# Kernel optimization log

Hardware: AMD Instinct MI355X
Metric: run time of the kernel (lower is better)

The kernel has to match this reference:

```python
import jax, jax.numpy as jnp
import numpy as np

N_CLASSES = 256
GT_CLASSES = 21
DIM = 384
EPS = 1e-12  # matches torch F.normalize default eps


def setup_inputs() -> dict:
    key = jax.random.key(0)
    k1, k2, k3 = jax.random.split(key, 3)
    features = jax.random.normal(k1, (4, 256, 256, DIM), dtype=jnp.float32)
    weight = jax.random.uniform(k2, (4, 256, 256), dtype=jnp.float32)
    cluster_centers = jax.random.normal(k3, (N_CLASSES, DIM), dtype=jnp.float32)
    pseudo_assignment = (jnp.arange(N_CLASSES) % GT_CLASSES).astype(jnp.int32)
    return {
        "features": features,
        "weight": weight,
        "cluster_centers": cluster_centers,
        "pseudo_assignment": pseudo_assignment,
    }


def _l2norm(x, axis):
    # torch F.normalize: x / max(||x||, eps)
    n = jnp.sqrt(jnp.sum(x * x, axis=axis, keepdims=True))
    return x / jnp.maximum(n, EPS)


def reference(features, weight, cluster_centers, pseudo_assignment):
    lead_shape = features.shape[:-1]
    feats = features.reshape(-1, features.shape[-1])        # [N, D]
    w = weight.reshape(-1)                                   # [N]

    normed_clusters = _l2norm(cluster_centers, axis=1)       # [K, D]
    normed_features = _l2norm(feats, axis=1)                 # [N, D]

    inner_products = normed_features @ normed_clusters.T     # [N, K]
    class_labels = jnp.argmax(inner_products, axis=1)        # [N]

    # -(one_hot(labels) * inner_products).sum(1) == -inner_products[n, labels[n]]
    cluster_loss = -jnp.take_along_axis(
        inner_products, class_labels[:, None], axis=1
    )[:, 0]                                                  # [N]

    loss = jnp.mean(cluster_loss * w)

    pseudo_segs_pred = class_labels.reshape(lead_shape)
    segs_pred = pseudo_assignment[pseudo_segs_pred].astype(jnp.int64)
    return pseudo_segs_pred, segs_pred, loss
```

## Files before the change

### kernel.cpp

```cpp
#include <hip/hip_runtime.h>
#include <hip/hip_bf16.h>

#define NTOT (4*256*256)
#define DIM 384
#define KCL 256
#define BM 64
#define TBS 256
#define GRID_MAIN (NTOT/BM)
#define NT 12
#define EPS 1e-12f

#define AB(p) ((p) * 8192)
#define SMEM_BYTES 16384

typedef __attribute__((ext_vector_type(8))) _Float16 f16x8;
typedef __attribute__((ext_vector_type(4))) float f32x4;

__global__ void prep_clusters(const float* __restrict__ cc,
                              _Float16* __restrict__ bh,
                              _Float16* __restrict__ bl) {
    int j = blockIdx.x, l = threadIdx.x;
    float v[6]; float ssq = 0.f;
#pragma unroll
    for (int i = 0; i < 6; ++i) { v[i] = cc[j*DIM + l + 64*i]; ssq = fmaf(v[i], v[i], ssq); }
#pragma unroll
    for (int off = 32; off >= 1; off >>= 1) ssq += __shfl_xor(ssq, off);
    float inv = 1.f / fmaxf(sqrtf(ssq), EPS);
    const int w = j >> 6, n = (j >> 4) & 3, nl = j & 15;
#pragma unroll
    for (int i = 0; i < 6; ++i) {
        int d = l + 64 * i;
        float x = v[i] * inv;
        _Float16 h  = (_Float16)x;
        _Float16 lo = (_Float16)(x - (float)h);
        size_t idx = (size_t)((((((d >> 5)*4 + w)*4 + n)*4 + ((d >> 3) & 3))*16 + nl)*8
                              + (d & 7));
        bh[idx] = h;
        bl[idx] = lo;
    }
}

__global__ __launch_bounds__(TBS, 3)
void kmeans_main(const float* __restrict__ A,
                 const float* __restrict__ W,
                 const _Float16* __restrict__ Bh,
                 const _Float16* __restrict__ Bl,
                 const int*   __restrict__ PA,
                 float* __restrict__ out,
                 float* __restrict__ partial)
{
    __shared__ unsigned char smem[SMEM_BYTES];

    const int tid  = threadIdx.x;
    const int wv   = tid >> 6;
    const int lane = tid & 63;
    const int g    = lane >> 4;
    const int l15  = lane & 15;
    const int sw   = (l15 >> 1) & 3;
    const int row0 = blockIdx.x * BM;
    const int arow = tid >> 2, achk = tid & 3;
    const int awb  = (((arow << 2) + (achk ^ ((arow >> 1) & 3))) << 4);
    const int fa   = l15 * 64 + ((g ^ sw) << 4);

    const float* ap = A + (size_t)(row0 + arow) * DIM + achk * 8;
    const unsigned char* bsh = (const unsigned char*)Bh + (size_t)(wv * 4) * 1024 + lane * 16;
    const unsigned char* bsl = (const unsigned char*)Bl + (size_t)(wv * 4) * 1024 + lane * 16;

    f32x4 acc[4][4];
#pragma unroll
    for (int m = 0; m < 4; ++m)
#pragma unroll
        for (int n = 0; n < 4; ++n) acc[m][n] = (f32x4){0.f, 0.f, 0.f, 0.f};
    float ssq = 0.f;

    f16x8  bfh[4], bfl[4];
    float4 sA[2][2];

    auto LDA = [&](int s, int tt) {
        sA[s][0] = *(const float4*)(ap + tt * 32);
        sA[s][1] = *(const float4*)(ap + tt * 32 + 4);
    };
    auto LDBH = [&](int tt) {
#pragma unroll
        for (int n = 0; n < 4; ++n)
            bfh[n] = *(const f16x8*)(bsh + (size_t)(tt * 16 + n) * 1024);
    };
    auto LDBL = [&](int tt) {
#pragma unroll
        for (int n = 0; n < 4; ++n)
            bfl[n] = *(const f16x8*)(bsl + (size_t)(tt * 16 + n) * 1024);
    };
    auto CVTW = [&](int s, int p) {
        float av[8] = {sA[s][0].x, sA[s][0].y, sA[s][0].z, sA[s][0].w,
                       sA[s][1].x, sA[s][1].y, sA[s][1].z, sA[s][1].w};
        f16x8 h8, l8;
#pragma unroll
        for (int e = 0; e < 8; ++e) {
            _Float16 hh = (_Float16)av[e];
            h8[e] = hh;
            l8[e] = (_Float16)(av[e] - (float)hh);
            ssq = fmaf(av[e], av[e], ssq);
        }
        *(f16x8*)(smem + AB(p) + awb) = h8;
        *(f16x8*)(smem + AB(p) + 4096 + awb) = l8;
    };

    LDA(0, 0);
    LDBL(0); LDBH(0);
    LDA(1, 1);
    CVTW(0, 0);
    asm volatile("s_waitcnt lgkmcnt(0)" ::: "memory");
    __builtin_amdgcn_s_barrier();

#pragma unroll
    for (int t = 0; t < NT; ++t) {
        if (t + 2 < NT) LDA((t + 2) & 1, t + 2);

        f16x8 ahf[4], alf[4];
#pragma unroll
        for (int m = 0; m < 4; ++m) {
            ahf[m] = *(const f16x8*)(smem + AB(t & 1) + fa + m * 1024);
            alf[m] = *(const f16x8*)(smem + AB(t & 1) + 4096 + fa + m * 1024);
        }
        if (t + 1 < NT) CVTW((t + 1) & 1, (t + 1) & 1);
        asm volatile("s_waitcnt lgkmcnt(0)" ::: "memory");
        __builtin_amdgcn_s_barrier();

#pragma unroll
        for (int m = 0; m < 4; ++m)
#pragma unroll
            for (int n = 0; n < 4; ++n)
                acc[m][n] = __builtin_amdgcn_mfma_f32_16x16x32_f16(ahf[m], bfh[n], acc[m][n], 0, 0, 0);
#pragma unroll
        for (int m = 0; m < 4; ++m)
#pragma unroll
            for (int n = 0; n < 4; ++n)
                acc[m][n] = __builtin_amdgcn_mfma_f32_16x16x32_f16(ahf[m], bfl[n], acc[m][n], 0, 0, 0);
        if (t + 1 < NT) LDBL(t + 1);
#pragma unroll
        for (int m = 0; m < 4; ++m)
#pragma unroll
            for (int n = 0; n < 4; ++n)
                acc[m][n] = __builtin_amdgcn_mfma_f32_16x16x32_f16(alf[m], bfh[n], acc[m][n], 0, 0, 0);
        if (t + 1 < NT) LDBH(t + 1);
    }
    __syncthreads();

    float* rowssq = (float*)smem;
    float* wvalp  = (float*)(smem + 256);
    int*   wcolp  = (int*)(smem + 1280);

    ssq += __shfl_xor(ssq, 1);
    ssq += __shfl_xor(ssq, 2);
    if (achk == 0) rowssq[arow] = ssq;

#pragma unroll
    for (int m = 0; m < 4; ++m) {
#pragma unroll
        for (int j = 0; j < 4; ++j) {
            float best = acc[m][0][j];
            int   bc   = 64*wv + l15;
#pragma unroll
            for (int n = 1; n < 4; ++n) {
                float v = acc[m][n][j];
                int   c = 64*wv + 16*n + l15;
                if (v > best) { best = v; bc = c; }
            }
#pragma unroll
            for (int off = 1; off < 16; off <<= 1) {
                float ov = __shfl_xor(best, off);
                int   oc = __shfl_xor(bc, off);
                if (ov > best || (ov == best && oc < bc)) { best = ov; bc = oc; }
            }
            if (l15 == 0) {
                wvalp[wv * BM + 16*m + 4*g + j] = best;
                wcolp[wv * BM + 16*m + 4*g + j] = bc;
            }
        }
    }
    __syncthreads();

    if (tid < BM) {
        int r = tid;
        float best = wvalp[r]; int bc = wcolp[r];
#pragma unroll
        for (int w = 1; w < 4; ++w) {
            float ov = wvalp[w * BM + r]; int oc = wcolp[w * BM + r];
            if (ov > best || (ov == best && oc < bc)) { best = ov; bc = oc; }
        }
        float inv = 1.f / fmaxf(sqrtf(rowssq[r]), EPS);
        int gr = row0 + r;
        out[gr]        = (float)bc;
        out[NTOT + gr] = (float)PA[bc];
        float lsum = -(best * inv) * W[gr];
#pragma unroll
        for (int off = 32; off >= 1; off >>= 1) lsum += __shfl_xor(lsum, off);
        if (tid == 0) partial[blockIdx.x] = lsum;
    }
}

__global__ void loss_reduce(const float* __restrict__ partial, float* __restrict__ out_loss) {
    __shared__ float s[256];
    float v = 0.f;
    for (int i = threadIdx.x; i < GRID_MAIN; i += 256) v += partial[i];
    s[threadIdx.x] = v;
    __syncthreads();
    for (int off = 128; off >= 1; off >>= 1) {
        if ((int)threadIdx.x < off) s[threadIdx.x] += s[threadIdx.x + off];
        __syncthreads();
    }
    if (threadIdx.x == 0) out_loss[0] = s[0] * (1.0f / (float)NTOT);
}

extern "C" void kernel_launch(void* const* d_in, const int* in_sizes, int n_in,
                              void* d_out, int out_size, void* d_ws, size_t ws_size,
                              hipStream_t stream) {
    const float* features = (const float*)d_in[0];
    const float* weight   = (const float*)d_in[1];
    const float* cc       = (const float*)d_in[2];
    const int*   pa       = (const int*)d_in[3];
    float* out = (float*)d_out;

    _Float16* bh   = (_Float16*)d_ws;
    _Float16* bl   = bh + KCL * DIM;
    float* partial = (float*)(bl + KCL * DIM);

    hipLaunchKernelGGL(prep_clusters, dim3(KCL), dim3(64), 0, stream, cc, bh, bl);
    hipLaunchKernelGGL(kmeans_main, dim3(GRID_MAIN), dim3(TBS), 0, stream,
                       features, weight, bh, bl, pa, out, partial);
    hipLaunchKernelGGL(loss_reduce, dim3(1), dim3(256), 0, stream, partial, out + 2 * NTOT);
}
```

Before: 186.1 us.

## Give each wave a private LDS A tile and drop block barriers in main loop

The work split changes so that each wave computes a 32-row by 128-cluster tile instead of sharing a 64-row A tile across four waves. Each wave now loads, splits into fp16 hi/lo parts and stages its own rows in a private double-buffered LDS region, so the per-iteration block-wide barriers go away. B fragments are loaded per 4-column chunk inside the loop rather than prefetched a step ahead. The cost is that each A row is now fetched and converted by two waves, which doubles that global/L2 traffic and conversion work and doubles LDS use. B loads are also exposed with less latency hiding.

After: 234.7 us. +26.1%, slower.

```diff
diff --git a/kernel.cpp b/kernel.cpp
--- a/kernel.cpp
+++ b/kernel.cpp
@@ -10,8 +10,7 @@
 #define NT 12
 #define EPS 1e-12f
 
-#define AB(p) ((p) * 8192)
-#define SMEM_BYTES 16384
+#define SMEM_BYTES 32768
 
 typedef __attribute__((ext_vector_type(8))) _Float16 f16x8;
 typedef __attribute__((ext_vector_type(4))) float f32x4;
@@ -51,119 +50,125 @@
 {
     __shared__ unsigned char smem[SMEM_BYTES];
 
-    const int tid  = threadIdx.x;
-    const int wv   = tid >> 6;
-    const int lane = tid & 63;
-    const int g    = lane >> 4;
-    const int l15  = lane & 15;
-    const int sw   = (l15 >> 1) & 3;
-    const int row0 = blockIdx.x * BM;
-    const int arow = tid >> 2, achk = tid & 3;
-    const int awb  = (((arow << 2) + (achk ^ ((arow >> 1) & 3))) << 4);
-    const int fa   = l15 * 64 + ((g ^ sw) << 4);
-
-    const float* ap = A + (size_t)(row0 + arow) * DIM + achk * 8;
-    const unsigned char* bsh = (const unsigned char*)Bh + (size_t)(wv * 4) * 1024 + lane * 16;
-    const unsigned char* bsl = (const unsigned char*)Bl + (size_t)(wv * 4) * 1024 + lane * 16;
-
-    f32x4 acc[4][4];
-#pragma unroll
-    for (int m = 0; m < 4; ++m)
-#pragma unroll
-        for (int n = 0; n < 4; ++n) acc[m][n] = (f32x4){0.f, 0.f, 0.f, 0.f};
+    const int tid   = threadIdx.x;
+    const int wv    = tid >> 6;
+    const int lane  = tid & 63;
+    const int g     = lane >> 4;
+    const int l15   = lane & 15;
+    const int sw    = (l15 >> 1) & 3;
+    const int rstrip= wv >> 1;
+    const int chalf = wv & 1;
+    const int row0  = blockIdx.x * BM + rstrip * 32;
+
+    const int srow = lane >> 1;
+    const int shalf= lane & 1;
+    const float* ap = A + (size_t)(row0 + srow) * DIM + shalf * 16;
+
+    unsigned char* wbase = smem + wv * 8192;
+    const int wsw  = (srow >> 1) & 3;
+    const int ws0  = (srow * 4 + ((2 * shalf + 0) ^ wsw)) * 16;
+    const int ws1  = (srow * 4 + ((2 * shalf + 1) ^ wsw)) * 16;
+    const int fa   = (l15 * 4 + (g ^ sw)) * 16;
+
+    const unsigned char* bsh = (const unsigned char*)Bh + (size_t)(8 * chalf) * 1024 + lane * 16;
+    const unsigned char* bsl = (const unsigned char*)Bl + (size_t)(8 * chalf) * 1024 + lane * 16;
+
+    f32x4 acc[2][8];
+#pragma unroll
+    for (int m = 0; m < 2; ++m)
+#pragma unroll
+        for (int T = 0; T < 8; ++T) acc[m][T] = (f32x4){0.f, 0.f, 0.f, 0.f};
     float ssq = 0.f;
 
-    f16x8  bfh[4], bfl[4];
-    float4 sA[2][2];
+    float4 sA[2][4];
 
     auto LDA = [&](int s, int tt) {
-        sA[s][0] = *(const float4*)(ap + tt * 32);
-        sA[s][1] = *(const float4*)(ap + tt * 32 + 4);
-    };
-    auto LDBH = [&](int tt) {
-#pragma unroll
-        for (int n = 0; n < 4; ++n)
-            bfh[n] = *(const f16x8*)(bsh + (size_t)(tt * 16 + n) * 1024);
-    };
-    auto LDBL = [&](int tt) {
-#pragma unroll
-        for (int n = 0; n < 4; ++n)
-            bfl[n] = *(const f16x8*)(bsl + (size_t)(tt * 16 + n) * 1024);
+#pragma unroll
+        for (int q = 0; q < 4; ++q)
+            sA[s][q] = *(const float4*)(ap + tt * 32 + q * 4);
     };
     auto CVTW = [&](int s, int p) {
-        float av[8] = {sA[s][0].x, sA[s][0].y, sA[s][0].z, sA[s][0].w,
-                       sA[s][1].x, sA[s][1].y, sA[s][1].z, sA[s][1].w};
-        f16x8 h8, l8;
+        float f[16];
+#pragma unroll
+        for (int q = 0; q < 4; ++q) {
+            f[q*4+0] = sA[s][q].x; f[q*4+1] = sA[s][q].y;
+            f[q*4+2] = sA[s][q].z; f[q*4+3] = sA[s][q].w;
+        }
+        f16x8 h0, h1, l0, l1;
 #pragma unroll
         for (int e = 0; e < 8; ++e) {
-            _Float16 hh = (_Float16)av[e];
-            h8[e] = hh;
-            l8[e] = (_Float16)(av[e] - (float)hh);
-            ssq = fmaf(av[e], av[e], ssq);
-        }
-        *(f16x8*)(smem + AB(p) + awb) = h8;
-        *(f16x8*)(smem + AB(p) + 4096 + awb) = l8;
+            _Float16 hh = (_Float16)f[e];
+            h0[e] = hh; l0[e] = (_Float16)(f[e] - (float)hh);
+            ssq = fmaf(f[e], f[e], ssq);
+            _Float16 hh2 = (_Float16)f[8+e];
+            h1[e] = hh2; l1[e] = (_Float16)(f[8+e] - (float)hh2);
+            ssq = fmaf(f[8+e], f[8+e], ssq);
+        }
+        *(f16x8*)(wbase + p * 4096 + ws0)        = h0;
+        *(f16x8*)(wbase + p * 4096 + ws1)        = h1;
+        *(f16x8*)(wbase + p * 4096 + 2048 + ws0) = l0;
+        *(f16x8*)(wbase + p * 4096 + 2048 + ws1) = l1;
     };
 
     LDA(0, 0);
-    LDBL(0); LDBH(0);
     LDA(1, 1);
     CVTW(0, 0);
-    asm volatile("s_waitcnt lgkmcnt(0)" ::: "memory");
-    __builtin_amdgcn_s_barrier();
 
 #pragma unroll
     for (int t = 0; t < NT; ++t) {
-        if (t + 2 < NT) LDA((t + 2) & 1, t + 2);
-
-        f16x8 ahf[4], alf[4];
-#pragma unroll
-        for (int m = 0; m < 4; ++m) {
-            ahf[m] = *(const f16x8*)(smem + AB(t & 1) + fa + m * 1024);
-            alf[m] = *(const f16x8*)(smem + AB(t & 1) + 4096 + fa + m * 1024);
-        }
+        f16x8 ahf[2], alf[2];
+#pragma unroll
+        for (int m = 0; m < 2; ++m) {
+            ahf[m] = *(const f16x8*)(wbase + (t & 1) * 4096 + fa + m * 1024);
+            alf[m] = *(const f16x8*)(wbase + (t & 1) * 4096 + 2048 + fa + m * 1024);
+        }
+        if (t + 2 < NT) LDA(t & 1, t + 2);
         if (t + 1 < NT) CVTW((t + 1) & 1, (t + 1) & 1);
-        asm volatile("s_waitcnt lgkmcnt(0)" ::: "memory");
-        __builtin_amdgcn_s_barrier();
-
-#pragma unroll
-        for (int m = 0; m < 4; ++m)
-#pragma unroll
-            for (int n = 0; n < 4; ++n)
-                acc[m][n] = __builtin_amdgcn_mfma_f32_16x16x32_f16(ahf[m], bfh[n], acc[m][n], 0, 0, 0);
-#pragma unroll
-        for (int m = 0; m < 4; ++m)
-#pragma unroll
-            for (int n = 0; n < 4; ++n)
-                acc[m][n] = __builtin_amdgcn_mfma_f32_16x16x32_f16(ahf[m], bfl[n], acc[m][n], 0, 0, 0);
-        if (t + 1 < NT) LDBL(t + 1);
-#pragma unroll
-        for (int m = 0; m < 4; ++m)
-#pragma unroll
-            for (int n = 0; n < 4; ++n)
-                acc[m][n] = __builtin_amdgcn_mfma_f32_16x16x32_f16(alf[m], bfh[n], acc[m][n], 0, 0, 0);
-        if (t + 1 < NT) LDBH(t + 1);
-    }
+
+#pragma unroll
+        for (int ch = 0; ch < 2; ++ch) {
+            f16x8 bfh[4], bfl[4];
+#pragma unroll
+            for (int i = 0; i < 4; ++i) {
+                bfh[i] = *(const f16x8*)(bsh + (size_t)(t * 16 + ch * 4 + i) * 1024);
+                bfl[i] = *(const f16x8*)(bsl + (size_t)(t * 16 + ch * 4 + i) * 1024);
+            }
+#pragma unroll
+            for (int m = 0; m < 2; ++m)
+#pragma unroll
+                for (int i = 0; i < 4; ++i)
+                    acc[m][ch*4+i] = __builtin_amdgcn_mfma_f32_16x16x32_f16(ahf[m], bfh[i], acc[m][ch*4+i], 0, 0, 0);
+#pragma unroll
+            for (int m = 0; m < 2; ++m)
+#pragma unroll
+                for (int i = 0; i < 4; ++i)
+                    acc[m][ch*4+i] = __builtin_amdgcn_mfma_f32_16x16x32_f16(ahf[m], bfl[i], acc[m][ch*4+i], 0, 0, 0);
+#pragma unroll
+            for (int m = 0; m < 2; ++m)
+#pragma unroll
+                for (int i = 0; i < 4; ++i)
+                    acc[m][ch*4+i] = __builtin_amdgcn_mfma_f32_16x16x32_f16(alf[m], bfh[i], acc[m][ch*4+i], 0, 0, 0);
+        }
+    }
+
+    float* wvalp  = (float*)smem;
+    int*   wcolp  = (int*)(smem + 512);
+    float* rowssq = (float*)(smem + 1024);
     __syncthreads();
 
-    float* rowssq = (float*)smem;
-    float* wvalp  = (float*)(smem + 256);
-    int*   wcolp  = (int*)(smem + 1280);
-
     ssq += __shfl_xor(ssq, 1);
-    ssq += __shfl_xor(ssq, 2);
-    if (achk == 0) rowssq[arow] = ssq;
-
-#pragma unroll
-    for (int m = 0; m < 4; ++m) {
+    if (chalf == 0 && shalf == 0) rowssq[rstrip * 32 + srow] = ssq;
+
+#pragma unroll
+    for (int m = 0; m < 2; ++m) {
 #pragma unroll
         for (int j = 0; j < 4; ++j) {
             float best = acc[m][0][j];
-            int   bc   = 64*wv + l15;
-#pragma unroll
-            for (int n = 1; n < 4; ++n) {
-                float v = acc[m][n][j];
-                int   c = 64*wv + 16*n + l15;
+            int   bc   = 128 * chalf + l15;
+#pragma unroll
+            for (int T = 1; T < 8; ++T) {
+                float v = acc[m][T][j];
+                int   c = 128 * chalf + 16 * T + l15;
                 if (v > best) { best = v; bc = c; }
             }
 #pragma unroll
@@ -173,8 +178,9 @@
                 if (ov > best || (ov == best && oc < bc)) { best = ov; bc = oc; }
             }
             if (l15 == 0) {
-                wvalp[wv * BM + 16*m + 4*g + j] = best;
-                wcolp[wv * BM + 16*m + 4*g + j] = bc;
+                int rl = 16 * m + 4 * g + j;
+                wvalp[wv * 32 + rl] = best;
+                wcolp[wv * 32 + rl] = bc;
             }
         }
     }
@@ -182,17 +188,17 @@
 
     if (tid < BM) {
         int r = tid;
-        float best = wvalp[r]; int bc = wcolp[r];
-#pragma unroll
-        for (int w = 1; w < 4; ++w) {
-            float ov = wvalp[w * BM + r]; int oc = wcolp[w * BM + r];
-            if (ov > best || (ov == best && oc < bc)) { best = ov; bc = oc; }
-        }
+        int w0 = (r >> 5) * 2;
+        int rl = r & 31;
+        float b0 = wvalp[w0 * 32 + rl];      int c0 = wcolp[w0 * 32 + rl];
+        float b1 = wvalp[(w0 + 1) * 32 + rl]; int c1 = wcolp[(w0 + 1) * 32 + rl];
+        float b = b0; int c = c0;
+        if (b1 > b) { b = b1; c = c1; }
         float inv = 1.f / fmaxf(sqrtf(rowssq[r]), EPS);
-        int gr = row0 + r;
-        out[gr]        = (float)bc;
-        out[NTOT + gr] = (float)PA[bc];
-        float lsum = -(best * inv) * W[gr];
+        int gr = blockIdx.x * BM + r;
+        out[gr]        = (float)c;
+        out[NTOT + gr] = (float)PA[c];
+        float lsum = -(b * inv) * W[gr];
 #pragma unroll
         for (int off = 32; off >= 1; off >>= 1) lsum += __shfl_xor(lsum, off);
         if (tid == 0) partial[blockIdx.x] = lsum;
```
